# Optimization experiments

Measured on AMD Instinct MI355X. Metric: run time of the kernel, lower is better.

The kernel has to match this reference:

```python
import jax, jax.numpy as jnp
import numpy as np

EMB = 768
B, LD, LW, LH = 2, 8, 8, 8        # LR grid = number of windows per axis
HD, HW, HH = 32, 32, 32           # HR volume
LN_EPS = 1e-5


def setup_inputs() -> dict:
    key = jax.random.key(0)
    ks = jax.random.split(key, 12)
    s = 1.0 / np.sqrt(EMB)
    inp = {
        "LR_image": jax.random.normal(ks[0], (B, LD, LW, LH, EMB), jnp.float32),
        "HR_image": jax.random.normal(ks[1], (B, HD, HW, HH, EMB), jnp.float32),
        "Wq_w": jax.random.uniform(ks[2], (EMB, EMB), jnp.float32, -s, s),
        "Wq_b": jax.random.uniform(ks[3], (EMB,), jnp.float32, -s, s),
        "Wk_w": jax.random.uniform(ks[4], (EMB, EMB), jnp.float32, -s, s),
        "Wk_b": jax.random.uniform(ks[5], (EMB,), jnp.float32, -s, s),
        "Wv_w": jax.random.uniform(ks[6], (EMB, EMB), jnp.float32, -s, s),
        "Wv_b": jax.random.uniform(ks[7], (EMB,), jnp.float32, -s, s),
        "Wo_w": jax.random.uniform(ks[8], (EMB, EMB), jnp.float32, -s, s),
        "Wo_b": jax.random.uniform(ks[9], (EMB,), jnp.float32, -s, s),
        "ln_g": jnp.ones((EMB,), jnp.float32),
        "ln_b": jnp.zeros((EMB,), jnp.float32),
        "S_d": 4, "S_w": 4, "S_h": 4,
    }
    return inp


def _window_partition(x, S_d, S_w, S_h):
    # x: [B, D, W, H, C] -> [B, N_blocks, S_d*S_w*S_h, C]
    b, d, w, h, c = x.shape
    x = x.reshape(b, d // S_d, S_d, w // S_w, S_w, h // S_h, S_h, c)
    x = jnp.transpose(x, (0, 2, 4, 6, 1, 3, 5, 7))  # [B,Sd,Sw,Sh,Db,Wb,Hb,C]
    x = x.reshape(b, S_d * S_w * S_h, -1, c)
    return jnp.transpose(x, (0, 2, 1, 3))  # [B, N_blocks, S, C]


def reference(LR_image, HR_image, Wq_w, Wq_b, Wk_w, Wk_b, Wv_w, Wv_b,
              Wo_w, Wo_b, ln_g, ln_b, S_d, S_w, S_h):
    b = LR_image.shape[0]
    c = LR_image.shape[-1]
    # queries: [B, N, 1, C]
    q_in = LR_image.reshape(b, -1, c)[:, :, None, :]
    # windowed keys/values: [B, N, S, C]
    hr = _window_partition(HR_image, S_d, S_w, S_h)
    q = q_in @ Wq_w.T + Wq_b
    k = hr @ Wk_w.T + Wk_b
    v = hr @ Wv_w.T + Wv_b
    scale = 1.0 / jnp.sqrt(jnp.asarray(c, q.dtype))
    scores = jnp.einsum('bnqc,bnsc->bnqs', q, k) * scale  # [B,N,1,S]
    attn = jax.nn.softmax(scores, axis=-1)
    x = jnp.einsum('bnqs,bnsc->bnqc', attn, v).reshape(b, -1, c)
    x = x @ Wo_w.T + Wo_b
    res = q.reshape(b, -1, c) + x  # residual with projected queries
    mu = jnp.mean(res, axis=-1, keepdims=True)
    var = jnp.var(res, axis=-1, keepdims=True)
    return (res - mu) / jnp.sqrt(var + LN_EPS) * ln_g + ln_b
```

## Files before the change

### kernel.cpp

```cpp
#include <hip/hip_runtime.h>
#include <hip/hip_bf16.h>
#include <math.h>

#define EMB 768
#define NB 2
#define NWIN 512
#define NROWS (NB*NWIN)
#define SWIN 64
#define HRDIM 32
#define ROWF (NROWS*EMB)
#define WELEM (EMB*EMB)

using bfrag = __attribute__((ext_vector_type(8))) short;
using f32x4 = __attribute__((ext_vector_type(4))) float;

#define GL16(g, l)  __builtin_amdgcn_global_load_lds(                         \
    (const __attribute__((address_space(1))) void*)(g),                       \
    (__attribute__((address_space(3))) void*)(l), 16, 0, 0)

__global__ __launch_bounds__(256)
void f2b3_kernel(const float* __restrict__ iA, __hip_bfloat16* __restrict__ oA, int nA,
                 const float* __restrict__ iB, __hip_bfloat16* __restrict__ oB, int nB,
                 const float* __restrict__ iC, __hip_bfloat16* __restrict__ oC, int nC) {
  const float* in; __hip_bfloat16* out; int n8;
  if (blockIdx.y == 0)      { in = iA; out = oA; n8 = nA; }
  else if (blockIdx.y == 1) { in = iB; out = oB; n8 = nB; }
  else                      { in = iC; out = oC; n8 = nC; }
  int i = blockIdx.x * 256 + threadIdx.x;
  if (i >= n8) return;
  float4 a = *(const float4*)&in[(size_t)i * 8];
  float4 b = *(const float4*)&in[(size_t)i * 8 + 4];
  __hip_bfloat16 t[8];
  t[0] = __float2bfloat16(a.x); t[1] = __float2bfloat16(a.y);
  t[2] = __float2bfloat16(a.z); t[3] = __float2bfloat16(a.w);
  t[4] = __float2bfloat16(b.x); t[5] = __float2bfloat16(b.y);
  t[6] = __float2bfloat16(b.z); t[7] = __float2bfloat16(b.w);
  *(uint4*)&out[(size_t)i * 8] = *(const uint4*)t;
}

__global__ __launch_bounds__(256)
void f2bT3_kernel(const float* __restrict__ iA, __hip_bfloat16* __restrict__ oA,
                  const float* __restrict__ iB, __hip_bfloat16* __restrict__ oB,
                  const float* __restrict__ iC, __hip_bfloat16* __restrict__ oC) {
  const float* in; __hip_bfloat16* out;
  if (blockIdx.z == 0)      { in = iA; out = oA; }
  else if (blockIdx.z == 1) { in = iB; out = oB; }
  else                      { in = iC; out = oC; }
  __shared__ float tile[32][33];
  const int bi = blockIdx.x, bj = blockIdx.y;
  const int c = threadIdx.x & 31, r8 = threadIdx.x >> 5;
#pragma unroll
  for (int rr = 0; rr < 4; ++rr) {
    int r = r8 + rr * 8;
    tile[c][r] = in[(size_t)(bi * 32 + r) * EMB + bj * 32 + c];
  }
  __syncthreads();
#pragma unroll
  for (int rr = 0; rr < 4; ++rr) {
    int n = r8 + rr * 8;
    out[(size_t)(bj * 32 + n) * EMB + bi * 32 + c] = __float2bfloat16(tile[n][c]);
  }
}

__global__ __launch_bounds__(256)
void bias_kernel(const float* __restrict__ bq, const float* __restrict__ Wk,
                 const float* __restrict__ Wo, const float* __restrict__ bv,
                 const float* __restrict__ bo, float* __restrict__ bqk,
                 float* __restrict__ bvo) {
  const int t = threadIdx.x;
  if (blockIdx.x < 12) {
    __shared__ float red[4][64];
    const int io = t & 63, cg = t >> 6;
    const int i = blockIdx.x * 64 + io;
    float s = 0.f;
#pragma unroll 8
    for (int c = cg; c < EMB; c += 4)
      s = fmaf(bq[c], Wk[(size_t)c * EMB + i], s);
    red[cg][io] = s;
    __syncthreads();
    if (cg == 0)
      bqk[i] = red[0][io] + red[1][io] + red[2][io] + red[3][io];
  } else {
    const int w = t >> 6, lane = t & 63;
    const int p = (blockIdx.x - 12) * 4 + w;
    float s = 0.f;
#pragma unroll
    for (int r = 0; r < 12; ++r) {
      int n = lane + r * 64;
      s = fmaf(Wo[(size_t)p * EMB + n], bv[n], s);
    }
#pragma unroll
    for (int o = 32; o > 0; o >>= 1) s += __shfl_xor(s, o, 64);
    if (lane == 0) bvo[p] = bo[p] + s;
  }
}

template<bool BIAS, bool WF32, bool WB16>
__global__ __launch_bounds__(256)
void gemm_bf16(const __hip_bfloat16* __restrict__ A0,
               const __hip_bfloat16* __restrict__ A1,
               const __hip_bfloat16* __restrict__ B0,
               const __hip_bfloat16* __restrict__ B1,
               const float* __restrict__ bias0, const float* __restrict__ bias1,
               float* __restrict__ Cf0, float* __restrict__ Cf1,
               __hip_bfloat16* __restrict__ Cb0, __hip_bfloat16* __restrict__ Cb1,
               int N) {
  constexpr int K = EMB;
  constexpr int NT = K / 64;
  const int zi = blockIdx.z;
  const __hip_bfloat16* A  = zi ? A1 : A0;
  const __hip_bfloat16* Bm = zi ? B1 : B0;
  const float* bias = zi ? bias1 : bias0;
  float* Cf = zi ? Cf1 : Cf0;
  __hip_bfloat16* Cb = zi ? Cb1 : Cb0;

  __shared__ short lsA[3][64 * 64];
  __shared__ short lsB[3][64 * 64];
  const int t = threadIdx.x;
  const int w = t >> 6, lane = t & 63;
  const int lr = lane & 15, lk = lane >> 4;
  const int m0 = blockIdx.y * 64, n0 = blockIdx.x * 64;

  const int r0 = t >> 3, c0 = t & 7;
  const int kc = c0 ^ (r0 & 7);
  const __hip_bfloat16* aptr0 = A + (size_t)(m0 + r0) * K + kc * 8;
  const __hip_bfloat16* aptr1 = A + (size_t)(m0 + r0 + 32) * K + kc * 8;
  const __hip_bfloat16* bptr0 = Bm + (size_t)(n0 + r0) * K + kc * 8;
  const __hip_bfloat16* bptr1 = Bm + (size_t)(n0 + r0 + 32) * K + kc * 8;
  const int wbase = w * 512;

  const int arow = w * 16 + lr;
  int aoff[2], boff[4][2];
#pragma unroll
  for (int ks = 0; ks < 2; ++ks)
    aoff[ks] = arow * 64 + (((ks << 2) | lk) ^ (arow & 7)) * 8;
#pragma unroll
  for (int f = 0; f < 4; ++f) {
    int br = f * 16 + lr;
#pragma unroll
    for (int ks = 0; ks < 2; ++ks)
      boff[f][ks] = br * 64 + (((ks << 2) | lk) ^ (br & 7)) * 8;
  }

  f32x4 acc[4];
#pragma unroll
  for (int f = 0; f < 4; ++f) acc[f] = (f32x4){0.f, 0.f, 0.f, 0.f};

#pragma unroll
  for (int p = 0; p < 2; ++p) {
    int ko = p * 64;
    GL16(aptr0 + ko, &lsA[p][wbase]);
    GL16(aptr1 + ko, &lsA[p][wbase + 2048]);
    GL16(bptr0 + ko, &lsB[p][wbase]);
    GL16(bptr1 + ko, &lsB[p][wbase + 2048]);
  }

#pragma unroll
  for (int kt = 0; kt < NT; ++kt) {
    if (kt + 2 < NT) {
      constexpr int s3[NT + 2] = {0,1,2,0,1,2,0,1,2,0,1,2,0,1};
      const int sl = s3[kt + 2];
      int ko = (kt + 2) * 64;
      GL16(aptr0 + ko, &lsA[sl][wbase]);
      GL16(aptr1 + ko, &lsA[sl][wbase + 2048]);
      GL16(bptr0 + ko, &lsB[sl][wbase]);
      GL16(bptr1 + ko, &lsB[sl][wbase + 2048]);
    }
    if (kt + 2 < NT)      asm volatile("s_waitcnt vmcnt(8)" ::: "memory");
    else if (kt + 1 < NT) asm volatile("s_waitcnt vmcnt(4)" ::: "memory");
    else                  asm volatile("s_waitcnt vmcnt(0)" ::: "memory");
    __builtin_amdgcn_sched_barrier(0);
    __builtin_amdgcn_s_barrier();

    const int cur = kt % 3;
    bfrag a0 = *(const bfrag*)&lsA[cur][aoff[0]];
    bfrag a1 = *(const bfrag*)&lsA[cur][aoff[1]];
    bfrag b00 = *(const bfrag*)&lsB[cur][boff[0][0]];
    bfrag b01 = *(const bfrag*)&lsB[cur][boff[0][1]];
    bfrag b10 = *(const bfrag*)&lsB[cur][boff[1][0]];
    bfrag b11 = *(const bfrag*)&lsB[cur][boff[1][1]];
    bfrag b20 = *(const bfrag*)&lsB[cur][boff[2][0]];
    bfrag b21 = *(const bfrag*)&lsB[cur][boff[2][1]];
    bfrag b30 = *(const bfrag*)&lsB[cur][boff[3][0]];
    bfrag b31 = *(const bfrag*)&lsB[cur][boff[3][1]];
    acc[0] = __builtin_amdgcn_mfma_f32_16x16x32_bf16(a0, b00, acc[0], 0, 0, 0);
    acc[0] = __builtin_amdgcn_mfma_f32_16x16x32_bf16(a1, b01, acc[0], 0, 0, 0);
    acc[1] = __builtin_amdgcn_mfma_f32_16x16x32_bf16(a0, b10, acc[1], 0, 0, 0);
    acc[1] = __builtin_amdgcn_mfma_f32_16x16x32_bf16(a1, b11, acc[1], 0, 0, 0);
    acc[2] = __builtin_amdgcn_mfma_f32_16x16x32_bf16(a0, b20, acc[2], 0, 0, 0);
    acc[2] = __builtin_amdgcn_mfma_f32_16x16x32_bf16(a1, b21, acc[2], 0, 0, 0);
    acc[3] = __builtin_amdgcn_mfma_f32_16x16x32_bf16(a0, b30, acc[3], 0, 0, 0);
    acc[3] = __builtin_amdgcn_mfma_f32_16x16x32_bf16(a1, b31, acc[3], 0, 0, 0);

    asm volatile("s_waitcnt lgkmcnt(0)" ::: "memory");
    __builtin_amdgcn_s_barrier();
    __builtin_amdgcn_sched_barrier(0);
  }

  float bs[4] = {0.f, 0.f, 0.f, 0.f};
  if (BIAS) {
#pragma unroll
    for (int f = 0; f < 4; ++f) bs[f] = bias[n0 + f * 16 + lr];
  }
#pragma unroll
  for (int f = 0; f < 4; ++f) {
    int n = n0 + f * 16 + lr;
#pragma unroll
    for (int j = 0; j < 4; ++j) {
      int m = m0 + w * 16 + lk * 4 + j;
      float v = acc[f][j] + bs[f];
      if (WF32) Cf[(size_t)m * N + n] = v;
      if (WB16) Cb[(size_t)m * N + n] = __float2bfloat16(v);
    }
  }
}

__global__ __launch_bounds__(512)
void attn_kernel(const float* __restrict__ HR, const float* __restrict__ qt,
                 __hip_bfloat16* __restrict__ zb) {
  const int g = blockIdx.x;
  const int b = g >> 9;
  const int n = g & 511;
  const int db = n >> 6, wb = (n >> 3) & 7, hb = n & 7;

  __shared__ float zp[8][EMB];
  __shared__ float ml[8][2];

  const int t = threadIdx.x;
  const int w = t >> 6, lane = t & 63;

  float4 qv[3];
#pragma unroll
  for (int r = 0; r < 3; ++r)
    qv[r] = *(const float4*)&qt[(size_t)g * EMB + (lane + r * 64) * 4];

  const float* rows[8];
#pragma unroll
  for (int i = 0; i < 8; ++i) {
    int s = w * 8 + i;
    int D = db * 4 + (s >> 4), W = wb * 4 + ((s >> 2) & 3), H = hb * 4 + (s & 3);
    rows[i] = HR + (size_t)((((b * HRDIM + D) * HRDIM + W) * HRDIM + H)) * EMB;
  }

  const float scale = 0.036084391824351615f;
  float m = -3.0e38f, l = 0.f;
  float4 z0 = {0,0,0,0}, z1 = {0,0,0,0}, z2 = {0,0,0,0};

  float4 h0 = *(const float4*)&rows[0][lane * 4];
  float4 h1 = *(const float4*)&rows[0][(lane + 64) * 4];
  float4 h2 = *(const float4*)&rows[0][(lane + 128) * 4];

#pragma unroll
  for (int i = 0; i < 8; ++i) {
    float4 n0, n1, n2;
    if (i < 7) {
      n0 = *(const float4*)&rows[i + 1][lane * 4];
      n1 = *(const float4*)&rows[i + 1][(lane + 64) * 4];
      n2 = *(const float4*)&rows[i + 1][(lane + 128) * 4];
    }
    float p = 0.f;
    p = fmaf(h0.x, qv[0].x, p); p = fmaf(h0.y, qv[0].y, p);
    p = fmaf(h0.z, qv[0].z, p); p = fmaf(h0.w, qv[0].w, p);
    p = fmaf(h1.x, qv[1].x, p); p = fmaf(h1.y, qv[1].y, p);
    p = fmaf(h1.z, qv[1].z, p); p = fmaf(h1.w, qv[1].w, p);
    p = fmaf(h2.x, qv[2].x, p); p = fmaf(h2.y, qv[2].y, p);
    p = fmaf(h2.z, qv[2].z, p); p = fmaf(h2.w, qv[2].w, p);
#pragma unroll
    for (int o = 32; o > 0; o >>= 1) p += __shfl_xor(p, o, 64);
    p *= scale;
    float mn = fmaxf(m, p);
    float f = expf(m - mn);
    float e = expf(p - mn);
    z0.x = fmaf(e, h0.x, z0.x * f); z0.y = fmaf(e, h0.y, z0.y * f);
    z0.z = fmaf(e, h0.z, z0.z * f); z0.w = fmaf(e, h0.w, z0.w * f);
    z1.x = fmaf(e, h1.x, z1.x * f); z1.y = fmaf(e, h1.y, z1.y * f);
    z1.z = fmaf(e, h1.z, z1.z * f); z1.w = fmaf(e, h1.w, z1.w * f);
    z2.x = fmaf(e, h2.x, z2.x * f); z2.y = fmaf(e, h2.y, z2.y * f);
    z2.z = fmaf(e, h2.z, z2.z * f); z2.w = fmaf(e, h2.w, z2.w * f);
    l = fmaf(l, f, e);
    m = mn;
    if (i < 7) { h0 = n0; h1 = n1; h2 = n2; }
  }

  *(float4*)&zp[w][lane * 4] = z0;
  *(float4*)&zp[w][(lane + 64) * 4] = z1;
  *(float4*)&zp[w][(lane + 128) * 4] = z2;
  if (lane == 0) { ml[w][0] = m; ml[w][1] = l; }
  __syncthreads();

  if (t < 384) {
    float M = -3.0e38f;
#pragma unroll
    for (int w8 = 0; w8 < 8; ++w8) M = fmaxf(M, ml[w8][0]);
    float L = 0.f, a0 = 0.f, a1 = 0.f;
#pragma unroll
    for (int w8 = 0; w8 < 8; ++w8) {
      float ew = expf(ml[w8][0] - M);
      L = fmaf(ml[w8][1], ew, L);
      float2 v = *(const float2*)&zp[w8][t * 2];
      a0 = fmaf(v.x, ew, a0);
      a1 = fmaf(v.y, ew, a1);
    }
    float rl = 1.f / L;
    __hip_bfloat16 o[2];
    o[0] = __float2bfloat16(a0 * rl);
    o[1] = __float2bfloat16(a1 * rl);
    *(unsigned*)&zb[(size_t)g * EMB + t * 2] = *(const unsigned*)o;
  }
}

__global__ __launch_bounds__(256)
void resid_ln_kernel(const float* __restrict__ Q, const float* __restrict__ X,
                     const float* __restrict__ gma, const float* __restrict__ bta,
                     float* __restrict__ out) {
  const int row = blockIdx.x;
  const int t = threadIdx.x;
  const int wave = t >> 6, lane = t & 63;
  __shared__ float red[4];

  float v[3];
  float s = 0.f;
#pragma unroll
  for (int r = 0; r < 3; ++r) {
    int c = t + r * 256;
    v[r] = Q[(size_t)row * EMB + c] + X[(size_t)row * EMB + c];
    s += v[r];
  }
#pragma unroll
  for (int o = 32; o > 0; o >>= 1) s += __shfl_xor(s, o, 64);
  if (lane == 0) red[wave] = s;
  __syncthreads();
  float mu = (red[0] + red[1] + red[2] + red[3]) * (1.f / EMB);
  __syncthreads();

  float q = 0.f;
#pragma unroll
  for (int r = 0; r < 3; ++r) {
    float d = v[r] - mu;
    q += d * d;
  }
#pragma unroll
  for (int o = 32; o > 0; o >>= 1) q += __shfl_xor(q, o, 64);
  if (lane == 0) red[wave] = q;
  __syncthreads();
  float var = (red[0] + red[1] + red[2] + red[3]) * (1.f / EMB);
  float inv = rsqrtf(var + 1e-5f);

#pragma unroll
  for (int r = 0; r < 3; ++r) {
    int c = t + r * 256;
    out[(size_t)row * EMB + c] = (v[r] - mu) * inv * gma[c] + bta[c];
  }
}

extern "C" void kernel_launch(void* const* d_in, const int* in_sizes, int n_in,
                              void* d_out, int out_size, void* d_ws, size_t ws_size,
                              hipStream_t stream) {
  const float* LR  = (const float*)d_in[0];
  const float* HR  = (const float*)d_in[1];
  const float* Wq  = (const float*)d_in[2];
  const float* bq  = (const float*)d_in[3];
  const float* Wk  = (const float*)d_in[4];
  const float* Wv  = (const float*)d_in[6];
  const float* bv  = (const float*)d_in[7];
  const float* Wo  = (const float*)d_in[8];
  const float* bo  = (const float*)d_in[9];
  const float* lng = (const float*)d_in[10];
  const float* lnb = (const float*)d_in[11];
  float* out = (float*)d_out;

  char* ws = (char*)d_ws;
  float* Qf = (float*)(ws + 0);
  float* qt = (float*)(ws + 3145728);
  float* x  = (float*)(ws + 6291456);
  __hip_bfloat16* LRb  = (__hip_bfloat16*)(ws +  9437184);
  __hip_bfloat16* zb   = (__hip_bfloat16*)(ws + 11010048);
  __hip_bfloat16* Wqb  = (__hip_bfloat16*)(ws + 12582912);
  __hip_bfloat16* Wob  = (__hip_bfloat16*)(ws + 13762560);
  __hip_bfloat16* WqTb = (__hip_bfloat16*)(ws + 14942208);
  __hip_bfloat16* WkTb = (__hip_bfloat16*)(ws + 16121856);
  __hip_bfloat16* WvTb = (__hip_bfloat16*)(ws + 17301504);
  __hip_bfloat16* Wqkb = (__hip_bfloat16*)(ws + 18481152);
  __hip_bfloat16* Wvob = (__hip_bfloat16*)(ws + 19660800);
  float* bqk = (float*)(ws + 20840448);
  float* bvo = (float*)(ws + 20843520);

  dim3 blk(256);

  f2b3_kernel<<<dim3(384, 3), blk, 0, stream>>>(
      LR, LRb, ROWF / 8, Wq, Wqb, WELEM / 8, Wo, Wob, WELEM / 8);
  f2bT3_kernel<<<dim3(24, 24, 3), blk, 0, stream>>>(
      Wq, WqTb, Wk, WkTb, Wv, WvTb);
  gemm_bf16<false, false, true><<<dim3(12, 12, 2), blk, 0, stream>>>(
      WkTb, Wob, WqTb, WvTb, nullptr, nullptr,
      nullptr, nullptr, Wqkb, Wvob, EMB);
  bias_kernel<<<dim3(204), blk, 0, stream>>>(bq, Wk, Wo, bv, bo, bqk, bvo);
  gemm_bf16<true, true, false><<<dim3(12, 16, 2), blk, 0, stream>>>(
      LRb, LRb, Wqb, Wqkb, bq, bqk, Qf, qt, nullptr, nullptr, EMB);
  attn_kernel<<<dim3(NROWS), dim3(512), 0, stream>>>(HR, qt, zb);
  gemm_bf16<true, true, false><<<dim3(12, 16, 1), blk, 0, stream>>>(
      zb, zb, Wvob, Wvob, bvo, bvo, x, x, nullptr, nullptr, EMB);
  resid_ln_kernel<<<dim3(NROWS), blk, 0, stream>>>(Qf, x, lng, lnb, out);
}
```

Baseline: 85.04 us.

## Merge prep kernels, enlarge GEMM tiles to 128x128, fuse residual into GEMM epilogue

Folds the three preprocessing kernels (bf16 casts, transposes, bias folding) into one launch. Replaces the 64x64 GEMM with a 128x128 tile in which each wave computes a 4x4 grid of MFMA fragments, for more data reuse per LDS load. Adds the residual Q to the output GEMM epilogue so the layernorm kernel reads one array instead of two. The larger tiles cut the grid to 36-96 blocks on a GPU with many CUs, so occupancy drops, and LDS use grows to 96KB per block.

After: 87.52 us. 1.03x slower.

```diff
diff --git a/kernel.cpp b/kernel.cpp
--- a/kernel.cpp
+++ b/kernel.cpp
@@ -19,92 +19,93 @@
     (__attribute__((address_space(3))) void*)(l), 16, 0, 0)
 
 __global__ __launch_bounds__(256)
-void f2b3_kernel(const float* __restrict__ iA, __hip_bfloat16* __restrict__ oA, int nA,
-                 const float* __restrict__ iB, __hip_bfloat16* __restrict__ oB, int nB,
-                 const float* __restrict__ iC, __hip_bfloat16* __restrict__ oC, int nC) {
-  const float* in; __hip_bfloat16* out; int n8;
-  if (blockIdx.y == 0)      { in = iA; out = oA; n8 = nA; }
-  else if (blockIdx.y == 1) { in = iB; out = oB; n8 = nB; }
-  else                      { in = iC; out = oC; n8 = nC; }
-  int i = blockIdx.x * 256 + threadIdx.x;
-  if (i >= n8) return;
-  float4 a = *(const float4*)&in[(size_t)i * 8];
-  float4 b = *(const float4*)&in[(size_t)i * 8 + 4];
-  __hip_bfloat16 t[8];
-  t[0] = __float2bfloat16(a.x); t[1] = __float2bfloat16(a.y);
-  t[2] = __float2bfloat16(a.z); t[3] = __float2bfloat16(a.w);
-  t[4] = __float2bfloat16(b.x); t[5] = __float2bfloat16(b.y);
-  t[6] = __float2bfloat16(b.z); t[7] = __float2bfloat16(b.w);
-  *(uint4*)&out[(size_t)i * 8] = *(const uint4*)t;
+void prep_kernel(const float* __restrict__ LR, __hip_bfloat16* __restrict__ LRb,
+                 const float* __restrict__ Wq, __hip_bfloat16* __restrict__ Wqb,
+                 const float* __restrict__ Wo, __hip_bfloat16* __restrict__ Wob,
+                 __hip_bfloat16* __restrict__ WqTb,
+                 const float* __restrict__ Wk, __hip_bfloat16* __restrict__ WkTb,
+                 const float* __restrict__ Wv, __hip_bfloat16* __restrict__ WvTb,
+                 const float* __restrict__ bq, const float* __restrict__ bv,
+                 const float* __restrict__ bo,
+                 float* __restrict__ bqk, float* __restrict__ bvo) {
+  __shared__ float tile[32][33];
+  const int bx = blockIdx.x;
+  const int t = threadIdx.x;
+
+  if (bx < 960) {
+    const float* in; __hip_bfloat16* out; int i;
+    if (bx < 384)      { in = LR; out = LRb; i = bx * 256 + t; }
+    else if (bx < 672) { in = Wq; out = Wqb; i = (bx - 384) * 256 + t; }
+    else               { in = Wo; out = Wob; i = (bx - 672) * 256 + t; }
+    float4 a = *(const float4*)&in[(size_t)i * 8];
+    float4 b = *(const float4*)&in[(size_t)i * 8 + 4];
+    __hip_bfloat16 o[8];
+    o[0] = __float2bfloat16(a.x); o[1] = __float2bfloat16(a.y);
+    o[2] = __float2bfloat16(a.z); o[3] = __float2bfloat16(a.w);
+    o[4] = __float2bfloat16(b.x); o[5] = __float2bfloat16(b.y);
+    o[6] = __float2bfloat16(b.z); o[7] = __float2bfloat16(b.w);
+    *(uint4*)&out[(size_t)i * 8] = *(const uint4*)o;
+  } else if (bx < 2688) {
+    int idx = bx - 960;
+    int z = idx / 576, rem = idx % 576;
+    int bi = rem % 24, bj = rem / 24;
+    const float* in; __hip_bfloat16* out;
+    if (z == 0)      { in = Wq; out = WqTb; }
+    else if (z == 1) { in = Wk; out = WkTb; }
+    else             { in = Wv; out = WvTb; }
+    const int c = t & 31, r8 = t >> 5;
+#pragma unroll
+    for (int rr = 0; rr < 4; ++rr) {
+      int r = r8 + rr * 8;
+      tile[c][r] = in[(size_t)(bi * 32 + r) * EMB + bj * 32 + c];
+    }
+    __syncthreads();
+#pragma unroll
+    for (int rr = 0; rr < 4; ++rr) {
+      int n = r8 + rr * 8;
+      out[(size_t)(bj * 32 + n) * EMB + bi * 32 + c] = __float2bfloat16(tile[n][c]);
+    }
+  } else {
+    int idx = bx - 2688;
+    if (idx < 12) {
+      __shared__ float red[4][64];
+      const int io = t & 63, cg = t >> 6;
+      const int i = idx * 64 + io;
+      float s = 0.f;
+#pragma unroll 8
+      for (int c = cg; c < EMB; c += 4)
+        s = fmaf(bq[c], Wk[(size_t)c * EMB + i], s);
+      red[cg][io] = s;
+      __syncthreads();
+      if (cg == 0)
+        bqk[i] = red[0][io] + red[1][io] + red[2][io] + red[3][io];
+    } else {
+      const int w = t >> 6, lane = t & 63;
+      const int p = (idx - 12) * 4 + w;
+      float s = 0.f;
+#pragma unroll
+      for (int r = 0; r < 12; ++r) {
+        int n = lane + r * 64;
+        s = fmaf(Wo[(size_t)p * EMB + n], bv[n], s);
+      }
+#pragma unroll
+      for (int o = 32; o > 0; o >>= 1) s += __shfl_xor(s, o, 64);
+      if (lane == 0) bvo[p] = bo[p] + s;
+    }
+  }
 }
 
+template<bool BIAS, bool WF32, bool WB16, bool RESID>
 __global__ __launch_bounds__(256)
-void f2bT3_kernel(const float* __restrict__ iA, __hip_bfloat16* __restrict__ oA,
-                  const float* __restrict__ iB, __hip_bfloat16* __restrict__ oB,
-                  const float* __restrict__ iC, __hip_bfloat16* __restrict__ oC) {
-  const float* in; __hip_bfloat16* out;
-  if (blockIdx.z == 0)      { in = iA; out = oA; }
-  else if (blockIdx.z == 1) { in = iB; out = oB; }
-  else                      { in = iC; out = oC; }
-  __shared__ float tile[32][33];
-  const int bi = blockIdx.x, bj = blockIdx.y;
-  const int c = threadIdx.x & 31, r8 = threadIdx.x >> 5;
-#pragma unroll
-  for (int rr = 0; rr < 4; ++rr) {
-    int r = r8 + rr * 8;
-    tile[c][r] = in[(size_t)(bi * 32 + r) * EMB + bj * 32 + c];
-  }
-  __syncthreads();
-#pragma unroll
-  for (int rr = 0; rr < 4; ++rr) {
-    int n = r8 + rr * 8;
-    out[(size_t)(bj * 32 + n) * EMB + bi * 32 + c] = __float2bfloat16(tile[n][c]);
-  }
-}
-
-__global__ __launch_bounds__(256)
-void bias_kernel(const float* __restrict__ bq, const float* __restrict__ Wk,
-                 const float* __restrict__ Wo, const float* __restrict__ bv,
-                 const float* __restrict__ bo, float* __restrict__ bqk,
-                 float* __restrict__ bvo) {
-  const int t = threadIdx.x;
-  if (blockIdx.x < 12) {
-    __shared__ float red[4][64];
-    const int io = t & 63, cg = t >> 6;
-    const int i = blockIdx.x * 64 + io;
-    float s = 0.f;
-#pragma unroll 8
-    for (int c = cg; c < EMB; c += 4)
-      s = fmaf(bq[c], Wk[(size_t)c * EMB + i], s);
-    red[cg][io] = s;
-    __syncthreads();
-    if (cg == 0)
-      bqk[i] = red[0][io] + red[1][io] + red[2][io] + red[3][io];
-  } else {
-    const int w = t >> 6, lane = t & 63;
-    const int p = (blockIdx.x - 12) * 4 + w;
-    float s = 0.f;
-#pragma unroll
-    for (int r = 0; r < 12; ++r) {
-      int n = lane + r * 64;
-      s = fmaf(Wo[(size_t)p * EMB + n], bv[n], s);
-    }
-#pragma unroll
-    for (int o = 32; o > 0; o >>= 1) s += __shfl_xor(s, o, 64);
-    if (lane == 0) bvo[p] = bo[p] + s;
-  }
-}
-
-template<bool BIAS, bool WF32, bool WB16>
-__global__ __launch_bounds__(256)
-void gemm_bf16(const __hip_bfloat16* __restrict__ A0,
-               const __hip_bfloat16* __restrict__ A1,
-               const __hip_bfloat16* __restrict__ B0,
-               const __hip_bfloat16* __restrict__ B1,
-               const float* __restrict__ bias0, const float* __restrict__ bias1,
-               float* __restrict__ Cf0, float* __restrict__ Cf1,
-               __hip_bfloat16* __restrict__ Cb0, __hip_bfloat16* __restrict__ Cb1,
-               int N) {
+void gemm128(const __hip_bfloat16* __restrict__ A0,
+             const __hip_bfloat16* __restrict__ A1,
+             const __hip_bfloat16* __restrict__ B0,
+             const __hip_bfloat16* __restrict__ B1,
+             const float* __restrict__ bias0, const float* __restrict__ bias1,
+             float* __restrict__ Cf0, float* __restrict__ Cf1,
+             __hip_bfloat16* __restrict__ Cb0, __hip_bfloat16* __restrict__ Cb1,
+             const float* __restrict__ R0, const float* __restrict__ R1,
+             int N) {
   constexpr int K = EMB;
   constexpr int NT = K / 64;
   const int zi = blockIdx.z;
@@ -113,104 +114,108 @@
   const float* bias = zi ? bias1 : bias0;
   float* Cf = zi ? Cf1 : Cf0;
   __hip_bfloat16* Cb = zi ? Cb1 : Cb0;
-
-  __shared__ short lsA[3][64 * 64];
-  __shared__ short lsB[3][64 * 64];
+  const float* R = zi ? R1 : R0;
+
+  __shared__ short lsA[3][128 * 64];
+  __shared__ short lsB[3][128 * 64];
   const int t = threadIdx.x;
   const int w = t >> 6, lane = t & 63;
   const int lr = lane & 15, lk = lane >> 4;
-  const int m0 = blockIdx.y * 64, n0 = blockIdx.x * 64;
-
-  const int r0 = t >> 3, c0 = t & 7;
-  const int kc = c0 ^ (r0 & 7);
-  const __hip_bfloat16* aptr0 = A + (size_t)(m0 + r0) * K + kc * 8;
-  const __hip_bfloat16* aptr1 = A + (size_t)(m0 + r0 + 32) * K + kc * 8;
-  const __hip_bfloat16* bptr0 = Bm + (size_t)(n0 + r0) * K + kc * 8;
-  const __hip_bfloat16* bptr1 = Bm + (size_t)(n0 + r0 + 32) * K + kc * 8;
-  const int wbase = w * 512;
-
-  const int arow = w * 16 + lr;
-  int aoff[2], boff[4][2];
-#pragma unroll
-  for (int ks = 0; ks < 2; ++ks)
-    aoff[ks] = arow * 64 + (((ks << 2) | lk) ^ (arow & 7)) * 8;
+  const int wr = w >> 1, wc = w & 1;
+  const int m0 = blockIdx.y * 128, n0 = blockIdx.x * 128;
+
+  const int r0 = t >> 3;
+  const int kc = (t & 7) ^ (r0 & 7);
+  const __hip_bfloat16* aptr = A + (size_t)(m0 + r0) * K + kc * 8;
+  const __hip_bfloat16* bptr = Bm + (size_t)(n0 + r0) * K + kc * 8;
+  const int wb512 = w * 512;
+
+#define STAGE128(sl, ko)                                                      \
+  do {                                                                        \
+    GL16(aptr + 0 * 32 * K + (ko), &lsA[sl][0 * 2048 + wb512]);               \
+    GL16(aptr + 1 * 32 * K + (ko), &lsA[sl][1 * 2048 + wb512]);               \
+    GL16(aptr + 2 * 32 * K + (ko), &lsA[sl][2 * 2048 + wb512]);               \
+    GL16(aptr + 3 * 32 * K + (ko), &lsA[sl][3 * 2048 + wb512]);               \
+    GL16(bptr + 0 * 32 * K + (ko), &lsB[sl][0 * 2048 + wb512]);               \
+    GL16(bptr + 1 * 32 * K + (ko), &lsB[sl][1 * 2048 + wb512]);               \
+    GL16(bptr + 2 * 32 * K + (ko), &lsB[sl][2 * 2048 + wb512]);               \
+    GL16(bptr + 3 * 32 * K + (ko), &lsB[sl][3 * 2048 + wb512]);               \
+  } while (0)
+
+  int aoff[4][2], boff[4][2];
 #pragma unroll
   for (int f = 0; f < 4; ++f) {
-    int br = f * 16 + lr;
-#pragma unroll
-    for (int ks = 0; ks < 2; ++ks)
-      boff[f][ks] = br * 64 + (((ks << 2) | lk) ^ (br & 7)) * 8;
-  }
-
-  f32x4 acc[4];
-#pragma unroll
-  for (int f = 0; f < 4; ++f) acc[f] = (f32x4){0.f, 0.f, 0.f, 0.f};
-
-#pragma unroll
-  for (int p = 0; p < 2; ++p) {
-    int ko = p * 64;
-    GL16(aptr0 + ko, &lsA[p][wbase]);
-    GL16(aptr1 + ko, &lsA[p][wbase + 2048]);
-    GL16(bptr0 + ko, &lsB[p][wbase]);
-    GL16(bptr1 + ko, &lsB[p][wbase + 2048]);
-  }
+    int ar = wr * 64 + f * 16 + lr;
+    int br = wc * 64 + f * 16 + lr;
+#pragma unroll
+    for (int ks = 0; ks < 2; ++ks) {
+      aoff[f][ks] = ar * 64 + ((((ks << 2) | lk) ^ (ar & 7)) << 3);
+      boff[f][ks] = br * 64 + ((((ks << 2) | lk) ^ (br & 7)) << 3);
+    }
+  }
+
+  f32x4 acc[4][4];
+#pragma unroll
+  for (int i = 0; i < 4; ++i)
+#pragma unroll
+    for (int j = 0; j < 4; ++j) acc[i][j] = (f32x4){0.f, 0.f, 0.f, 0.f};
+
+  STAGE128(0, 0);
+  STAGE128(1, 64);
 
 #pragma unroll
   for (int kt = 0; kt < NT; ++kt) {
     if (kt + 2 < NT) {
       constexpr int s3[NT + 2] = {0,1,2,0,1,2,0,1,2,0,1,2,0,1};
-      const int sl = s3[kt + 2];
-      int ko = (kt + 2) * 64;
-      GL16(aptr0 + ko, &lsA[sl][wbase]);
-      GL16(aptr1 + ko, &lsA[sl][wbase + 2048]);
-      GL16(bptr0 + ko, &lsB[sl][wbase]);
-      GL16(bptr1 + ko, &lsB[sl][wbase + 2048]);
-    }
-    if (kt + 2 < NT)      asm volatile("s_waitcnt vmcnt(8)" ::: "memory");
-    else if (kt + 1 < NT) asm volatile("s_waitcnt vmcnt(4)" ::: "memory");
+      STAGE128(s3[kt + 2], (kt + 2) * 64);
+    }
+    if (kt + 2 < NT)      asm volatile("s_waitcnt vmcnt(16)" ::: "memory");
+    else if (kt + 1 < NT) asm volatile("s_waitcnt vmcnt(8)" ::: "memory");
     else                  asm volatile("s_waitcnt vmcnt(0)" ::: "memory");
     __builtin_amdgcn_sched_barrier(0);
     __builtin_amdgcn_s_barrier();
 
     const int cur = kt % 3;
-    bfrag a0 = *(const bfrag*)&lsA[cur][aoff[0]];
-    bfrag a1 = *(const bfrag*)&lsA[cur][aoff[1]];
-    bfrag b00 = *(const bfrag*)&lsB[cur][boff[0][0]];
-    bfrag b01 = *(const bfrag*)&lsB[cur][boff[0][1]];
-    bfrag b10 = *(const bfrag*)&lsB[cur][boff[1][0]];
-    bfrag b11 = *(const bfrag*)&lsB[cur][boff[1][1]];
-    bfrag b20 = *(const bfrag*)&lsB[cur][boff[2][0]];
-    bfrag b21 = *(const bfrag*)&lsB[cur][boff[2][1]];
-    bfrag b30 = *(const bfrag*)&lsB[cur][boff[3][0]];
-    bfrag b31 = *(const bfrag*)&lsB[cur][boff[3][1]];
-    acc[0] = __builtin_amdgcn_mfma_f32_16x16x32_bf16(a0, b00, acc[0], 0, 0, 0);
-    acc[0] = __builtin_amdgcn_mfma_f32_16x16x32_bf16(a1, b01, acc[0], 0, 0, 0);
-    acc[1] = __builtin_amdgcn_mfma_f32_16x16x32_bf16(a0, b10, acc[1], 0, 0, 0);
-    acc[1] = __builtin_amdgcn_mfma_f32_16x16x32_bf16(a1, b11, acc[1], 0, 0, 0);
-    acc[2] = __builtin_amdgcn_mfma_f32_16x16x32_bf16(a0, b20, acc[2], 0, 0, 0);
-    acc[2] = __builtin_amdgcn_mfma_f32_16x16x32_bf16(a1, b21, acc[2], 0, 0, 0);
-    acc[3] = __builtin_amdgcn_mfma_f32_16x16x32_bf16(a0, b30, acc[3], 0, 0, 0);
-    acc[3] = __builtin_amdgcn_mfma_f32_16x16x32_bf16(a1, b31, acc[3], 0, 0, 0);
+#pragma unroll
+    for (int ks = 0; ks < 2; ++ks) {
+      bfrag a_[4], b_[4];
+#pragma unroll
+      for (int f = 0; f < 4; ++f) {
+        a_[f] = *(const bfrag*)&lsA[cur][aoff[f][ks]];
+        b_[f] = *(const bfrag*)&lsB[cur][boff[f][ks]];
+      }
+#pragma unroll
+      for (int i = 0; i < 4; ++i)
+#pragma unroll
+        for (int j = 0; j < 4; ++j)
+          acc[i][j] = __builtin_amdgcn_mfma_f32_16x16x32_bf16(
+              a_[i], b_[j], acc[i][j], 0, 0, 0);
+    }
 
     asm volatile("s_waitcnt lgkmcnt(0)" ::: "memory");
     __builtin_amdgcn_s_barrier();
     __builtin_amdgcn_sched_barrier(0);
   }
-
-  float bs[4] = {0.f, 0.f, 0.f, 0.f};
-  if (BIAS) {
-#pragma unroll
-    for (int f = 0; f < 4; ++f) bs[f] = bias[n0 + f * 16 + lr];
-  }
-#pragma unroll
-  for (int f = 0; f < 4; ++f) {
-    int n = n0 + f * 16 + lr;
+#undef STAGE128
+
+  float bs[4];
+#pragma unroll
+  for (int j = 0; j < 4; ++j)
+    bs[j] = BIAS ? bias[n0 + wc * 64 + j * 16 + lr] : 0.f;
+
+#pragma unroll
+  for (int i = 0; i < 4; ++i) {
 #pragma unroll
     for (int j = 0; j < 4; ++j) {
-      int m = m0 + w * 16 + lk * 4 + j;
-      float v = acc[f][j] + bs[f];
-      if (WF32) Cf[(size_t)m * N + n] = v;
-      if (WB16) Cb[(size_t)m * N + n] = __float2bfloat16(v);
+      int n = n0 + wc * 64 + j * 16 + lr;
+#pragma unroll
+      for (int q = 0; q < 4; ++q) {
+        int m = m0 + wr * 64 + i * 16 + lk * 4 + q;
+        float v = acc[i][j][q] + bs[j];
+        if (RESID) v += R[(size_t)m * N + n];
+        if (WF32) Cf[(size_t)m * N + n] = v;
+        if (WB16) Cb[(size_t)m * N + n] = __float2bfloat16(v);
+      }
     }
   }
 }
@@ -310,9 +315,8 @@
 }
 
 __global__ __launch_bounds__(256)
-void resid_ln_kernel(const float* __restrict__ Q, const float* __restrict__ X,
-                     const float* __restrict__ gma, const float* __restrict__ bta,
-                     float* __restrict__ out) {
+void ln_kernel(const float* __restrict__ R, const float* __restrict__ gma,
+               const float* __restrict__ bta, float* __restrict__ out) {
   const int row = blockIdx.x;
   const int t = threadIdx.x;
   const int wave = t >> 6, lane = t & 63;
@@ -323,7 +327,7 @@
 #pragma unroll
   for (int r = 0; r < 3; ++r) {
     int c = t + r * 256;
-    v[r] = Q[(size_t)row * EMB + c] + X[(size_t)row * EMB + c];
+    v[r] = R[(size_t)row * EMB + c];
     s += v[r];
   }
 #pragma unroll
@@ -387,18 +391,17 @@
 
   dim3 blk(256);
 
-  f2b3_kernel<<<dim3(384, 3), blk, 0, stream>>>(
-      LR, LRb, ROWF / 8, Wq, Wqb, WELEM / 8, Wo, Wob, WELEM / 8);
-  f2bT3_kernel<<<dim3(24, 24, 3), blk, 0, stream>>>(
-      Wq, WqTb, Wk, WkTb, Wv, WvTb);
-  gemm_bf16<false, false, true><<<dim3(12, 12, 2), blk, 0, stream>>>(
+  prep_kernel<<<dim3(2892), blk, 0, stream>>>(
+      LR, LRb, Wq, Wqb, Wo, Wob, WqTb, Wk, WkTb, Wv, WvTb,
+      bq, bv, bo, bqk, bvo);
+  gemm128<false, false, true, false><<<dim3(6, 6, 2), blk, 0, stream>>>(
       WkTb, Wob, WqTb, WvTb, nullptr, nullptr,
-      nullptr, nullptr, Wqkb, Wvob, EMB);
-  bias_kernel<<<dim3(204), blk, 0, stream>>>(bq, Wk, Wo, bv, bo, bqk, bvo);
-  gemm_bf16<true, true, false><<<dim3(12, 16, 2), blk, 0, stream>>>(
-      LRb, LRb, Wqb, Wqkb, bq, bqk, Qf, qt, nullptr, nullptr, EMB);
+      nullptr, nullptr, Wqkb, Wvob, nullptr, nullptr, EMB);
+  gemm128<true, true, false, false><<<dim3(6, 8, 2), blk, 0, stream>>>(
+      LRb, LRb, Wqb, Wqkb, bq, bqk, Qf, qt, nullptr, nullptr,
+      nullptr, nullptr, EMB);
   attn_kernel<<<dim3(NROWS), dim3(512), 0, stream>>>(HR, qt, zb);
-  gemm_bf16<true, true, false><<<dim3(12, 16, 1), blk, 0, stream>>>(
-      zb, zb, Wvob, Wvob, bvo, bvo, x, x, nullptr, nullptr, EMB);
-  resid_ln_kernel<<<dim3(NROWS), blk, 0, stream>>>(Qf, x, lng, lnb, out);
+  gemm128<true, true, false, true><<<dim3(6, 8, 1), blk, 0, stream>>>(
+      zb, zb, Wvob, Wvob, bvo, bvo, x, x, nullptr, nullptr, Qf, Qf, EMB);
+  ln_kernel<<<dim3(NROWS), blk, 0, stream>>>(x, lng, lnb, out);
 }
```
